# Performance work log

Hardware: AMD Instinct MI355X
Metric: run time of the kernel (lower is better)

## Reference

```python
import jax, jax.numpy as jnp
import numpy as np


def setup_inputs() -> dict:
    key = jax.random.key(0)
    k1, k2, k3 = jax.random.split(key, 3)
    B, T1, T2, D, MP = 16, 256, 256, 256, 32
    reps_lt = jax.random.normal(k1, (B, T1, D), dtype=jnp.float32)
    reps_rt = jax.random.normal(k2, (B, T2, D), dtype=jnp.float32)
    # keras 'uniform' initializer ~ U(-0.05, 0.05); stored as [mp, d]
    kernel = jax.random.uniform(k3, (MP, D), dtype=jnp.float32, minval=-0.05, maxval=0.05)
    return {"reps_lt": reps_lt, "reps_rt": reps_rt, "kernel": kernel}


def reference(reps_lt, reps_rt, kernel):
    # reps_lt: [b, t1, d], reps_rt: [b, t2, d], kernel: [mp, d]
    # Original: broadcast lt*kernel -> [b,t1,1,mp,d], rt -> [b,1,t2,1,d],
    # cosine_norm=False => tanh(sum over d), then max over t1.
    lt_m = reps_lt[:, :, None, :] * kernel[None, None, :, :]      # [b, t1, mp, d]
    scores = jnp.einsum('bimd,bjd->bijm', lt_m, reps_rt)           # [b, t1, t2, mp]
    match = jnp.tanh(scores)
    return jnp.max(match, axis=1)                                  # [b, t2, mp]
```

## Files before the change

### kernel.cpp

```cpp
#include <hip/hip_runtime.h>
#include <hip/hip_bf16.h>
#include <math.h>

#define Bn   16
#define T1n  256
#define T2n  256
#define Dn   256
#define MPn  32

typedef __attribute__((ext_vector_type(8)))  short short8;
typedef __attribute__((ext_vector_type(4)))  float f32x4;
typedef __attribute__((ext_vector_type(16))) float f32x16;

__device__ inline short f2b(float f) {
  __hip_bfloat16 h = __float2bfloat16(f);
  return __builtin_bit_cast(short, h);
}
__device__ inline float b2f(short s) {
  unsigned int u = ((unsigned int)(unsigned short)s) << 16;
  return __builtin_bit_cast(float, u);
}

__device__ inline int swz_chunk(int row, int d8) {
  return row * 32 + (d8 ^ (row & 7));
}

__global__ __launch_bounds__(256, 2)
void mp_match_kernel(const float* __restrict__ lt,
                     const float* __restrict__ rt,
                     const float* __restrict__ kern,
                     float* __restrict__ out) {
  __shared__ short lds_rt[64 * 256];
  __shared__ short lds_lt[64 * 256];

  const int bid = blockIdx.x;
  const int xcd = bid & 7;
  const int idx = bid >> 3;
  const int b   = ((idx >> 5) << 3) | xcd;
  const int rem = idx & 31;
  const int jblk = rem & 3;
  const int mg   = rem >> 2;
  const int j0   = jblk * 64;

  const int tid  = threadIdx.x;
  const int lane = tid & 63;
  const int w    = tid >> 6;
  const int m    = mg * 4 + w;
  const int l31  = lane & 31;
  const int kh   = lane >> 5;

  {
    const float* rbase = rt + ((size_t)b * T2n + j0) * Dn;
    #pragma unroll
    for (int rep = 0; rep < 8; ++rep) {
      int chunk = rep * 256 + tid;
      int row = chunk >> 5, c = chunk & 31;
      const f32x4* s = reinterpret_cast<const f32x4*>(rbase + row * Dn + c * 8);
      f32x4 f0 = s[0], f1 = s[1];
      short8 v;
      v[0] = f2b(f0.x); v[1] = f2b(f0.y); v[2] = f2b(f0.z); v[3] = f2b(f0.w);
      v[4] = f2b(f1.x); v[5] = f2b(f1.y); v[6] = f2b(f1.z); v[7] = f2b(f1.w);
      *reinterpret_cast<short8*>(&lds_rt[swz_chunk(row, c) * 8]) = v;
    }
  }
  __syncthreads();

  short8 bsc[2][16];
  {
    const float* kbase = kern + (size_t)m * Dn;
    #pragma unroll
    for (int ks = 0; ks < 16; ++ks) {
      int d8 = ks * 2 + kh;
      const f32x4* kp = reinterpret_cast<const f32x4*>(kbase + d8 * 8);
      f32x4 k0 = kp[0], k1 = kp[1];
      #pragma unroll
      for (int jf = 0; jf < 2; ++jf) {
        int brow = jf * 32 + l31;
        short8 r = *reinterpret_cast<const short8*>(&lds_rt[swz_chunk(brow, d8) * 8]);
        short8 v;
        v[0] = f2b(b2f(r[0]) * k0.x); v[1] = f2b(b2f(r[1]) * k0.y);
        v[2] = f2b(b2f(r[2]) * k0.z); v[3] = f2b(b2f(r[3]) * k0.w);
        v[4] = f2b(b2f(r[4]) * k1.x); v[5] = f2b(b2f(r[5]) * k1.y);
        v[6] = f2b(b2f(r[6]) * k1.z); v[7] = f2b(b2f(r[7]) * k1.w);
        bsc[jf][ks] = v;
      }
    }
  }

  float jmax0 = -1e30f, jmax1 = -1e30f;

  for (int ic = 0; ic < 4; ++ic) {
    if (ic) __syncthreads();
    const float* lbase = lt + ((size_t)b * T1n + ic * 64) * Dn;
    #pragma unroll
    for (int rep = 0; rep < 8; ++rep) {
      int chunk = rep * 256 + tid;
      int row = chunk >> 5, c = chunk & 31;
      const f32x4* s = reinterpret_cast<const f32x4*>(lbase + row * Dn + c * 8);
      f32x4 f0 = s[0], f1 = s[1];
      short8 v;
      v[0] = f2b(f0.x); v[1] = f2b(f0.y); v[2] = f2b(f0.z); v[3] = f2b(f0.w);
      v[4] = f2b(f1.x); v[5] = f2b(f1.y); v[6] = f2b(f1.z); v[7] = f2b(f1.w);
      *reinterpret_cast<short8*>(&lds_lt[swz_chunk(row, c) * 8]) = v;
    }
    __syncthreads();

    f32x16 c00 = {}, c01 = {}, c10 = {}, c11 = {};
    #pragma unroll
    for (int ks = 0; ks < 16; ++ks) {
      int d8 = ks * 2 + kh;
      short8 A0 = *reinterpret_cast<const short8*>(&lds_lt[swz_chunk(l31, d8) * 8]);
      short8 A1 = *reinterpret_cast<const short8*>(&lds_lt[swz_chunk(32 + l31, d8) * 8]);
      c00 = __builtin_amdgcn_mfma_f32_32x32x16_bf16(A0, bsc[0][ks], c00, 0, 0, 0);
      c01 = __builtin_amdgcn_mfma_f32_32x32x16_bf16(A0, bsc[1][ks], c01, 0, 0, 0);
      c10 = __builtin_amdgcn_mfma_f32_32x32x16_bf16(A1, bsc[0][ks], c10, 0, 0, 0);
      c11 = __builtin_amdgcn_mfma_f32_32x32x16_bf16(A1, bsc[1][ks], c11, 0, 0, 0);
    }
    #pragma unroll
    for (int r = 0; r < 16; ++r) {
      jmax0 = fmaxf(jmax0, fmaxf(c00[r], c10[r]));
      jmax1 = fmaxf(jmax1, fmaxf(c01[r], c11[r]));
    }
  }

  jmax0 = fmaxf(jmax0, __shfl_xor(jmax0, 32));
  jmax1 = fmaxf(jmax1, __shfl_xor(jmax1, 32));
  float v = (lane < 32) ? jmax0 : jmax1;
  int j = j0 + lane;
  out[((size_t)b * T2n + j) * MPn + m] = tanhf(v);
}

extern "C" void kernel_launch(void* const* d_in, const int* in_sizes, int n_in,
                              void* d_out, int out_size, void* d_ws, size_t ws_size,
                              hipStream_t stream) {
  const float* lt   = (const float*)d_in[0];
  const float* rt   = (const float*)d_in[1];
  const float* kern = (const float*)d_in[2];
  float* out = (float*)d_out;

  dim3 grid(512);
  dim3 block(256);
  mp_match_kernel<<<grid, block, 0, stream>>>(lt, rt, kern, out);
}
```

Baseline: 26.80 us.

## Split j across 8 waves per block and switch to 16x16x32 MFMA

```diff
diff --git a/kernel.cpp b/kernel.cpp
--- a/kernel.cpp
+++ b/kernel.cpp
@@ -8,9 +8,8 @@
 #define Dn   256
 #define MPn  32
 
-typedef __attribute__((ext_vector_type(8)))  short short8;
-typedef __attribute__((ext_vector_type(4)))  float f32x4;
-typedef __attribute__((ext_vector_type(16))) float f32x16;
+typedef __attribute__((ext_vector_type(8))) short short8;
+typedef __attribute__((ext_vector_type(4))) float f32x4;
 
 __device__ inline short f2b(float f) {
   __hip_bfloat16 h = __float2bfloat16(f);
@@ -20,12 +19,15 @@
   unsigned int u = ((unsigned int)(unsigned short)s) << 16;
   return __builtin_bit_cast(float, u);
 }
+__device__ inline float max4(f32x4 a) {
+  return fmaxf(fmaxf(a.x, a.y), fmaxf(a.z, a.w));
+}
 
 __device__ inline int swz_chunk(int row, int d8) {
   return row * 32 + (d8 ^ (row & 7));
 }
 
-__global__ __launch_bounds__(256, 2)
+__global__ __launch_bounds__(512, 4)
 void mp_match_kernel(const float* __restrict__ lt,
                      const float* __restrict__ rt,
                      const float* __restrict__ kern,
@@ -45,15 +47,16 @@
   const int tid  = threadIdx.x;
   const int lane = tid & 63;
   const int w    = tid >> 6;
-  const int m    = mg * 4 + w;
-  const int l31  = lane & 31;
-  const int kh   = lane >> 5;
+  const int m    = mg * 4 + (w & 3);
+  const int jh   = w >> 2;
+  const int bl   = lane & 15;
+  const int hl   = lane >> 4;
 
   {
     const float* rbase = rt + ((size_t)b * T2n + j0) * Dn;
     #pragma unroll
-    for (int rep = 0; rep < 8; ++rep) {
-      int chunk = rep * 256 + tid;
+    for (int rep = 0; rep < 4; ++rep) {
+      int chunk = rep * 512 + tid;
       int row = chunk >> 5, c = chunk & 31;
       const f32x4* s = reinterpret_cast<const f32x4*>(rbase + row * Dn + c * 8);
       f32x4 f0 = s[0], f1 = s[1];
@@ -65,24 +68,24 @@
   }
   __syncthreads();
 
-  short8 bsc[2][16];
+  short8 bsc[2][8];
   {
     const float* kbase = kern + (size_t)m * Dn;
     #pragma unroll
-    for (int ks = 0; ks < 16; ++ks) {
-      int d8 = ks * 2 + kh;
+    for (int kk = 0; kk < 8; ++kk) {
+      int d8 = kk * 4 + hl;
       const f32x4* kp = reinterpret_cast<const f32x4*>(kbase + d8 * 8);
       f32x4 k0 = kp[0], k1 = kp[1];
       #pragma unroll
-      for (int jf = 0; jf < 2; ++jf) {
-        int brow = jf * 32 + l31;
+      for (int sub = 0; sub < 2; ++sub) {
+        int brow = jh * 32 + sub * 16 + bl;
         short8 r = *reinterpret_cast<const short8*>(&lds_rt[swz_chunk(brow, d8) * 8]);
         short8 v;
         v[0] = f2b(b2f(r[0]) * k0.x); v[1] = f2b(b2f(r[1]) * k0.y);
         v[2] = f2b(b2f(r[2]) * k0.z); v[3] = f2b(b2f(r[3]) * k0.w);
         v[4] = f2b(b2f(r[4]) * k1.x); v[5] = f2b(b2f(r[5]) * k1.y);
         v[6] = f2b(b2f(r[6]) * k1.z); v[7] = f2b(b2f(r[7]) * k1.w);
-        bsc[jf][ks] = v;
+        bsc[sub][kk] = v;
       }
     }
   }
@@ -93,8 +96,8 @@
     if (ic) __syncthreads();
     const float* lbase = lt + ((size_t)b * T1n + ic * 64) * Dn;
     #pragma unroll
-    for (int rep = 0; rep < 8; ++rep) {
-      int chunk = rep * 256 + tid;
+    for (int rep = 0; rep < 4; ++rep) {
+      int chunk = rep * 512 + tid;
       int row = chunk >> 5, c = chunk & 31;
       const f32x4* s = reinterpret_cast<const f32x4*>(lbase + row * Dn + c * 8);
       f32x4 f0 = s[0], f1 = s[1];
@@ -105,29 +108,32 @@
     }
     __syncthreads();
 
-    f32x16 c00 = {}, c01 = {}, c10 = {}, c11 = {};
     #pragma unroll
-    for (int ks = 0; ks < 16; ++ks) {
-      int d8 = ks * 2 + kh;
-      short8 A0 = *reinterpret_cast<const short8*>(&lds_lt[swz_chunk(l31, d8) * 8]);
-      short8 A1 = *reinterpret_cast<const short8*>(&lds_lt[swz_chunk(32 + l31, d8) * 8]);
-      c00 = __builtin_amdgcn_mfma_f32_32x32x16_bf16(A0, bsc[0][ks], c00, 0, 0, 0);
-      c01 = __builtin_amdgcn_mfma_f32_32x32x16_bf16(A0, bsc[1][ks], c01, 0, 0, 0);
-      c10 = __builtin_amdgcn_mfma_f32_32x32x16_bf16(A1, bsc[0][ks], c10, 0, 0, 0);
-      c11 = __builtin_amdgcn_mfma_f32_32x32x16_bf16(A1, bsc[1][ks], c11, 0, 0, 0);
-    }
-    #pragma unroll
-    for (int r = 0; r < 16; ++r) {
-      jmax0 = fmaxf(jmax0, fmaxf(c00[r], c10[r]));
-      jmax1 = fmaxf(jmax1, fmaxf(c01[r], c11[r]));
+    for (int it2 = 0; it2 < 4; ++it2) {
+      int arow = it2 * 16 + bl;
+      f32x4 a0 = {0.f, 0.f, 0.f, 0.f};
+      f32x4 a1 = {0.f, 0.f, 0.f, 0.f};
+      #pragma unroll
+      for (int kk = 0; kk < 8; ++kk) {
+        short8 A = *reinterpret_cast<const short8*>(
+            &lds_lt[swz_chunk(arow, kk * 4 + hl) * 8]);
+        a0 = __builtin_amdgcn_mfma_f32_16x16x32_bf16(A, bsc[0][kk], a0, 0, 0, 0);
+        a1 = __builtin_amdgcn_mfma_f32_16x16x32_bf16(A, bsc[1][kk], a1, 0, 0, 0);
+      }
+      jmax0 = fmaxf(jmax0, max4(a0));
+      jmax1 = fmaxf(jmax1, max4(a1));
     }
   }
 
+  jmax0 = fmaxf(jmax0, __shfl_xor(jmax0, 16));
   jmax0 = fmaxf(jmax0, __shfl_xor(jmax0, 32));
+  jmax1 = fmaxf(jmax1, __shfl_xor(jmax1, 16));
   jmax1 = fmaxf(jmax1, __shfl_xor(jmax1, 32));
-  float v = (lane < 32) ? jmax0 : jmax1;
-  int j = j0 + lane;
-  out[((size_t)b * T2n + j) * MPn + m] = tanhf(v);
+  if (hl < 2) {
+    float v = hl ? jmax1 : jmax0;
+    int j = j0 + jh * 32 + hl * 16 + bl;
+    out[((size_t)b * T2n + j) * MPn + m] = tanhf(v);
+  }
 }
 
 extern "C" void kernel_launch(void* const* d_in, const int* in_sizes, int n_in,
@@ -139,6 +145,6 @@
   float* out = (float*)d_out;
 
   dim3 grid(512);
-  dim3 block(256);
+  dim3 block(512);
   mp_match_kernel<<<grid, block, 0, stream>>>(lt, rt, kern, out);
 }
```

Measured after the change: 26.57 us. About the same (-0.9%).
